# Kernel optimization log

Hardware: AMD Instinct MI355X
Metric: run time of the kernel (lower is better)

## Reference

```python
import jax, jax.numpy as jnp
import numpy as np

BLOCK = 128  # block_size in the original module


def weight_dequant(weight, scale):
    # weight: [O, I] fp8 values (simulated float32); scale: [O//BLOCK, I//BLOCK] fp32
    O, I = weight.shape
    w = weight.reshape(O // BLOCK, BLOCK, I // BLOCK, BLOCK)
    w = w * scale[:, None, :, None]
    return w.reshape(O, I)


def setup_inputs() -> dict:
    key = jax.random.key(0)
    k1, k2, k3, k4 = jax.random.split(key, 4)
    B, S, IN, OUT = 2, 2048, 4096, 16384
    x = jax.random.normal(k1, (B, S, IN), dtype=jnp.float32)
    weight = jax.random.normal(k2, (OUT, IN), dtype=jnp.float32)
    scale = jax.random.uniform(k3, (OUT // BLOCK, IN // BLOCK), dtype=jnp.float32, minval=0.01, maxval=0.05)
    bias = jax.random.normal(k4, (OUT,), dtype=jnp.float32)
    return {"x": x, "weight": weight, "scale": scale, "bias": bias}


def reference(x, weight, scale, bias):
    # bf16 gemm_impl path: block-wise dequant of fp8 weight, then F.linear(x, W) + bias
    w = weight_dequant(weight, scale)          # [O, I]
    out = jnp.einsum('bsi,oi->bso', x, w)      # x @ W^T
    return out + bias
```

## Files before the change

### kernel.cpp

```cpp
#include <hip/hip_runtime.h>
#include <hip/hip_bf16.h>

#define M_DIM 4096
#define N_DIM 16384
#define K_DIM 4096

typedef __bf16 bf16x8 __attribute__((ext_vector_type(8)));
typedef float f32x4 __attribute__((ext_vector_type(4)));

__device__ __forceinline__ void gload16(const void* g, void* l) {
    __builtin_amdgcn_global_load_lds((__attribute__((address_space(1))) void*)g,
                                     (__attribute__((address_space(3))) void*)l, 16, 0, 0);
}

__global__ __launch_bounds__(256) void cvt_x_kernel(const float* __restrict__ x,
                                                    __hip_bfloat16* __restrict__ out,
                                                    int ngroups) {
    int i = blockIdx.x * blockDim.x + threadIdx.x;
    int stride = gridDim.x * blockDim.x;
    for (; i < ngroups; i += stride) {
        const float4* p = (const float4*)(x + (size_t)i * 8);
        float4 v0 = p[0];
        float4 v1 = p[1];
        bf16x8 r;
        r[0] = (__bf16)v0.x; r[1] = (__bf16)v0.y; r[2] = (__bf16)v0.z; r[3] = (__bf16)v0.w;
        r[4] = (__bf16)v1.x; r[5] = (__bf16)v1.y; r[6] = (__bf16)v1.z; r[7] = (__bf16)v1.w;
        *(bf16x8*)(out + (size_t)i * 8) = r;
    }
}

__global__ __launch_bounds__(256) void dequant_w_kernel(const float* __restrict__ w,
                                                        const float* __restrict__ scale,
                                                        __hip_bfloat16* __restrict__ out) {
    const int ngroups = N_DIM * (K_DIM / 8);
    int i = blockIdx.x * blockDim.x + threadIdx.x;
    int stride = gridDim.x * blockDim.x;
    for (; i < ngroups; i += stride) {
        int row = i >> 9;
        int cg  = i & 511;
        float s = scale[(row >> 7) * (K_DIM / 128) + (cg >> 4)];
        const float4* p = (const float4*)(w + (size_t)i * 8);
        float4 v0 = p[0];
        float4 v1 = p[1];
        bf16x8 r;
        r[0] = (__bf16)(v0.x * s); r[1] = (__bf16)(v0.y * s);
        r[2] = (__bf16)(v0.z * s); r[3] = (__bf16)(v0.w * s);
        r[4] = (__bf16)(v1.x * s); r[5] = (__bf16)(v1.y * s);
        r[6] = (__bf16)(v1.z * s); r[7] = (__bf16)(v1.w * s);
        *(bf16x8*)(out + (size_t)i * 8) = r;
    }
}

__global__ __launch_bounds__(512, 2)
void gemm_bf16_kernel(const __hip_bfloat16* __restrict__ A,
                      const __hip_bfloat16* __restrict__ Bw,
                      const float* __restrict__ bias,
                      float* __restrict__ C) {
    constexpr int Mtiles = M_DIM / 256;
    constexpr int Ntiles = N_DIM / 256;
    constexpr int nwg = Mtiles * Ntiles;

    int bid = blockIdx.x;
    int swz = (bid & 7) * (nwg >> 3) + (bid >> 3);
    int bm = swz % Mtiles;
    int bn = swz / Mtiles;

    __shared__ bf16x8 sA[2][2048];
    __shared__ bf16x8 sB[2][2048];

    const int t = threadIdx.x;
    const int l = t & 63;
    const int w = t >> 6;
    const int wm = w >> 2;
    const int wn = w & 3;

    const int lr = l & 15;
    const int lk = l >> 4;
    const int l7 = lr & 7;

    const int s0 = lk ^ l7;
    const int s1 = (4 + lk) ^ l7;

    const int srow = w * 8 + (l >> 3);
    const int scol = ((l & 7) ^ (l >> 3)) << 3;

    const size_t K = K_DIM;
    const __hip_bfloat16* aB = A  + (size_t)(bm * 256) * K + scol;
    const __hip_bfloat16* bB = Bw + (size_t)(bn * 256) * K + scol;

    f32x4 acc[8][4] = {};

    const int arow = (wm * 128 + lr) * 8;
    const int brow = (wn * 64 + lr) * 8;

    char* A0b = (char*)&sA[0][0] + w * 1024;
    char* B0b = (char*)&sB[0][0] + w * 1024;
    char* A1b = (char*)&sA[1][0] + w * 1024;
    char* B1b = (char*)&sB[1][0] + w * 1024;

#define SH(lbase, gptr)                                                         \
    do {                                                                        \
        gload16((gptr) + (size_t)srow * K, (lbase));                            \
        gload16((gptr) + (size_t)(64 + srow) * K, (lbase) + 8192);              \
    } while (0)

#define RD_A(dst, pa_, roff)                                                    \
    _Pragma("unroll")                                                           \
    for (int mi = 0; mi < 4; ++mi) {                                            \
        dst[mi][0] = (pa_)[arow + (roff) + mi * 128 + s0];                      \
        dst[mi][1] = (pa_)[arow + (roff) + mi * 128 + s1];                      \
    }

#define RD_B(dst, pb_, roff)                                                    \
    _Pragma("unroll")                                                           \
    for (int ni = 0; ni < 2; ++ni) {                                            \
        dst[ni][0] = (pb_)[brow + (roff) + ni * 128 + s0];                      \
        dst[ni][1] = (pb_)[brow + (roff) + ni * 128 + s1];                      \
    }

#define MM(mo, no, af, bf)                                                      \
    do {                                                                        \
        __builtin_amdgcn_s_setprio(1);                                          \
        _Pragma("unroll")                                                       \
        for (int s = 0; s < 2; ++s)                                             \
            _Pragma("unroll")                                                   \
            for (int mi = 0; mi < 4; ++mi)                                      \
                _Pragma("unroll")                                               \
                for (int ni = 0; ni < 2; ++ni)                                  \
                    acc[(mo) + mi][(no) + ni] =                                 \
                        __builtin_amdgcn_mfma_f32_16x16x32_bf16(                \
                            af[mi][s], bf[ni][s], acc[(mo) + mi][(no) + ni],    \
                            0, 0, 0);                                           \
        __builtin_amdgcn_s_setprio(0);                                          \
    } while (0)

#define BAR()   __builtin_amdgcn_s_barrier()
#define SBAR()  __builtin_amdgcn_sched_barrier(0)
#define LGKM0() do { asm volatile("s_waitcnt lgkmcnt(0)" ::: "memory"); SBAR(); } while (0)

    bf16x8 a03[4][2], a47[4][2], b01[2][2], b23[2][2];
    const bf16x8* pa0 = &sA[0][0];
    const bf16x8* pb0 = &sB[0][0];
    const bf16x8* pa1 = &sA[1][0];
    const bf16x8* pb1 = &sB[1][0];

    SH(A0b, aB);  SH(A0b + 16384, aB + (size_t)128 * K);
    SH(B0b, bB);  SH(B0b + 16384, bB + (size_t)128 * K);
    SH(B1b, bB + 64);  SH(B1b + 16384, bB + 64 + (size_t)128 * K);
    asm volatile("s_waitcnt vmcnt(4)" ::: "memory");
    BAR();

    #pragma unroll 1
    for (int p = 0; p < 32; ++p) {
        const bool last = (p == 31);
        const __hip_bfloat16* gAu  = aB + (size_t)(2 * p + 1) * 64;
        const __hip_bfloat16* gAt2 = aB + (size_t)(2 * p + 2) * 64;
        const __hip_bfloat16* gBt2 = bB + (size_t)(2 * p + 2) * 64;
        const __hip_bfloat16* gBt3 = bB + (size_t)(2 * p + 3) * 64;

        RD_A(a03, pa0, 0); RD_B(b01, pb0, 0);
        SH(A1b, gAu);
        asm volatile("s_waitcnt lgkmcnt(8)" ::: "memory");
        BAR();
        LGKM0();
        MM(0, 0, a03, b01);
        BAR();
        RD_B(b23, pb0, 256);
        SH(A1b + 16384, gAu + (size_t)128 * K);
        BAR();
        LGKM0();
        MM(0, 2, a03, b23);
        BAR();
        RD_A(a47, pa0, 512);
        if (!last) SH(B0b, gBt2);
        BAR();
        LGKM0();
        MM(4, 0, a47, b01);
        BAR();
        if (!last) {
            SH(B0b + 16384, gBt2 + (size_t)128 * K);
            asm volatile("s_waitcnt vmcnt(4)" ::: "memory");
        } else {
            asm volatile("s_waitcnt vmcnt(0)" ::: "memory");
        }
        BAR();
        SBAR();
        MM(4, 2, a47, b23);
        BAR();

        RD_A(a03, pa1, 0); RD_B(b01, pb1, 0);
        if (!last) SH(A0b, gAt2);
        asm volatile("s_waitcnt lgkmcnt(8)" ::: "memory");
        BAR();
        LGKM0();
        MM(0, 0, a03, b01);
        BAR();
        RD_B(b23, pb1, 256);
        if (!last) SH(A0b + 16384, gAt2 + (size_t)128 * K);
        BAR();
        LGKM0();
        MM(0, 2, a03, b23);
        BAR();
        RD_A(a47, pa1, 512);
        if (!last) SH(B1b, gBt3);
        BAR();
        LGKM0();
        MM(4, 0, a47, b01);
        BAR();
        if (!last) {
            SH(B1b + 16384, gBt3 + (size_t)128 * K);
            asm volatile("s_waitcnt vmcnt(4)" ::: "memory");
        }
        BAR();
        SBAR();
        MM(4, 2, a47, b23);
        if (!last) BAR();
    }
#undef SH
#undef RD_A
#undef RD_B
#undef MM
#undef BAR
#undef SBAR
#undef LGKM0

    const int crow0 = bm * 256 + wm * 128;
    const int ccol0 = bn * 256 + wn * 64;
    #pragma unroll
    for (int ni = 0; ni < 4; ++ni) {
        int col = ccol0 + ni * 16 + lr;
        float bv = bias[col];
        #pragma unroll
        for (int mi = 0; mi < 8; ++mi) {
            int rbase = crow0 + mi * 16 + lk * 4;
            #pragma unroll
            for (int j = 0; j < 4; ++j) {
                C[(size_t)(rbase + j) * N_DIM + col] = acc[mi][ni][j] + bv;
            }
        }
    }
}

__global__ __launch_bounds__(256)
void gemm_fallback(const float* __restrict__ X, const float* __restrict__ W,
                   const float* __restrict__ scale, const float* __restrict__ bias,
                   float* __restrict__ C) {
    int bm = blockIdx.x % (M_DIM / 64);
    int bn = blockIdx.x / (M_DIM / 64);
    __shared__ float sA[64][33];
    __shared__ float sB[64][33];
    int t = threadIdx.x;
    int tx = t & 15, ty = t >> 4;
    float acc[4][4] = {};
    for (int kt = 0; kt < K_DIM / 32; ++kt) {
        float s = scale[(bn >> 1) * (K_DIM / 128) + (kt >> 2)];
        #pragma unroll
        for (int i = 0; i < 8; ++i) {
            int idx = t + i * 256;
            int r = idx >> 5, c = idx & 31;
            sA[r][c] = X[(size_t)(bm * 64 + r) * K_DIM + kt * 32 + c];
            sB[r][c] = W[(size_t)(bn * 64 + r) * K_DIM + kt * 32 + c] * s;
        }
        __syncthreads();
        #pragma unroll
        for (int k = 0; k < 32; ++k) {
            float a[4], b[4];
            #pragma unroll
            for (int i = 0; i < 4; ++i) a[i] = sA[ty * 4 + i][k];
            #pragma unroll
            for (int j = 0; j < 4; ++j) b[j] = sB[tx * 4 + j][k];
            #pragma unroll
            for (int i = 0; i < 4; ++i)
                #pragma unroll
                for (int j = 0; j < 4; ++j) acc[i][j] += a[i] * b[j];
        }
        __syncthreads();
    }
    #pragma unroll
    for (int i = 0; i < 4; ++i)
        #pragma unroll
        for (int j = 0; j < 4; ++j) {
            int row = bm * 64 + ty * 4 + i;
            int col = bn * 64 + tx * 4 + j;
            C[(size_t)row * N_DIM + col] = acc[i][j] + bias[col];
        }
}

extern "C" void kernel_launch(void* const* d_in, const int* in_sizes, int n_in,
                              void* d_out, int out_size, void* d_ws, size_t ws_size,
                              hipStream_t stream) {
    const float* x     = (const float*)d_in[0];
    const float* wgt   = (const float*)d_in[1];
    const float* scale = (const float*)d_in[2];
    const float* bias  = (const float*)d_in[3];
    float* out = (float*)d_out;

    const size_t need = ((size_t)M_DIM * K_DIM + (size_t)N_DIM * K_DIM) * sizeof(__hip_bfloat16);
    if (ws_size >= need) {
        __hip_bfloat16* xbf = (__hip_bfloat16*)d_ws;
        __hip_bfloat16* wbf = xbf + (size_t)M_DIM * K_DIM;
        cvt_x_kernel<<<2048, 256, 0, stream>>>(x, xbf, M_DIM * K_DIM / 8);
        dequant_w_kernel<<<4096, 256, 0, stream>>>(wgt, scale, wbf);
        gemm_bf16_kernel<<<(M_DIM / 256) * (N_DIM / 256), 512, 0, stream>>>(xbf, wbf, bias, out);
    } else {
        gemm_fallback<<<(M_DIM / 64) * (N_DIM / 64), 256, 0, stream>>>(x, wgt, scale, bias, out);
    }
}
```

Baseline: 714.0 us.

## Switch GEMM to 32x32x16 MFMA tiles and merge prep kernels

The GEMM inner loop now issues 32x32x16 bf16 MFMAs on 32-row fragments instead of 16x16x32, with a new LDS swizzle (XOR with wave index) and a re-mapped fragment read pattern and epilogue. This cuts the MFMA instruction count and LDS reads per FLOP. The two preprocessing kernels are also merged into one launch, saving a kernel launch and tail. The changed swizzle and the output row mapping risk bank conflicts or indexing errors.

```diff
diff --git a/kernel.cpp b/kernel.cpp
--- a/kernel.cpp
+++ b/kernel.cpp
@@ -6,48 +6,48 @@
 #define K_DIM 4096
 
 typedef __bf16 bf16x8 __attribute__((ext_vector_type(8)));
-typedef float f32x4 __attribute__((ext_vector_type(4)));
+typedef float f32x16 __attribute__((ext_vector_type(16)));
 
 __device__ __forceinline__ void gload16(const void* g, void* l) {
     __builtin_amdgcn_global_load_lds((__attribute__((address_space(1))) void*)g,
                                      (__attribute__((address_space(3))) void*)l, 16, 0, 0);
 }
 
-__global__ __launch_bounds__(256) void cvt_x_kernel(const float* __restrict__ x,
-                                                    __hip_bfloat16* __restrict__ out,
-                                                    int ngroups) {
-    int i = blockIdx.x * blockDim.x + threadIdx.x;
-    int stride = gridDim.x * blockDim.x;
-    for (; i < ngroups; i += stride) {
-        const float4* p = (const float4*)(x + (size_t)i * 8);
-        float4 v0 = p[0];
-        float4 v1 = p[1];
-        bf16x8 r;
-        r[0] = (__bf16)v0.x; r[1] = (__bf16)v0.y; r[2] = (__bf16)v0.z; r[3] = (__bf16)v0.w;
-        r[4] = (__bf16)v1.x; r[5] = (__bf16)v1.y; r[6] = (__bf16)v1.z; r[7] = (__bf16)v1.w;
-        *(bf16x8*)(out + (size_t)i * 8) = r;
-    }
-}
-
-__global__ __launch_bounds__(256) void dequant_w_kernel(const float* __restrict__ w,
-                                                        const float* __restrict__ scale,
-                                                        __hip_bfloat16* __restrict__ out) {
-    const int ngroups = N_DIM * (K_DIM / 8);
-    int i = blockIdx.x * blockDim.x + threadIdx.x;
-    int stride = gridDim.x * blockDim.x;
-    for (; i < ngroups; i += stride) {
-        int row = i >> 9;
-        int cg  = i & 511;
-        float s = scale[(row >> 7) * (K_DIM / 128) + (cg >> 4)];
-        const float4* p = (const float4*)(w + (size_t)i * 8);
-        float4 v0 = p[0];
-        float4 v1 = p[1];
-        bf16x8 r;
-        r[0] = (__bf16)(v0.x * s); r[1] = (__bf16)(v0.y * s);
-        r[2] = (__bf16)(v0.z * s); r[3] = (__bf16)(v0.w * s);
-        r[4] = (__bf16)(v1.x * s); r[5] = (__bf16)(v1.y * s);
-        r[6] = (__bf16)(v1.z * s); r[7] = (__bf16)(v1.w * s);
-        *(bf16x8*)(out + (size_t)i * 8) = r;
+__global__ __launch_bounds__(256) void prep_kernel(const float* __restrict__ x,
+                                                   const float* __restrict__ wgt,
+                                                   const float* __restrict__ scale,
+                                                   __hip_bfloat16* __restrict__ xbf,
+                                                   __hip_bfloat16* __restrict__ wbf) {
+    int b = blockIdx.x;
+    if (b < 2048) {
+        const int ng = M_DIM * K_DIM / 8;
+        int i = b * 256 + threadIdx.x;
+        for (; i < ng; i += 2048 * 256) {
+            const float4* p = (const float4*)(x + (size_t)i * 8);
+            float4 v0 = p[0];
+            float4 v1 = p[1];
+            bf16x8 r;
+            r[0] = (__bf16)v0.x; r[1] = (__bf16)v0.y; r[2] = (__bf16)v0.z; r[3] = (__bf16)v0.w;
+            r[4] = (__bf16)v1.x; r[5] = (__bf16)v1.y; r[6] = (__bf16)v1.z; r[7] = (__bf16)v1.w;
+            *(bf16x8*)(xbf + (size_t)i * 8) = r;
+        }
+    } else {
+        const int ng = N_DIM * (K_DIM / 8);
+        int i = (b - 2048) * 256 + threadIdx.x;
+        for (; i < ng; i += 4096 * 256) {
+            int row = i >> 9;
+            int cg  = i & 511;
+            float s = scale[(row >> 7) * (K_DIM / 128) + (cg >> 4)];
+            const float4* p = (const float4*)(wgt + (size_t)i * 8);
+            float4 v0 = p[0];
+            float4 v1 = p[1];
+            bf16x8 r;
+            r[0] = (__bf16)(v0.x * s); r[1] = (__bf16)(v0.y * s);
+            r[2] = (__bf16)(v0.z * s); r[3] = (__bf16)(v0.w * s);
+            r[4] = (__bf16)(v1.x * s); r[5] = (__bf16)(v1.y * s);
+            r[6] = (__bf16)(v1.z * s); r[7] = (__bf16)(v1.w * s);
+            *(bf16x8*)(wbf + (size_t)i * 8) = r;
+        }
     }
 }
 
@@ -74,24 +74,24 @@
     const int wm = w >> 2;
     const int wn = w & 3;
 
-    const int lr = l & 15;
-    const int lk = l >> 4;
-    const int l7 = lr & 7;
-
-    const int s0 = lk ^ l7;
-    const int s1 = (4 + lk) ^ l7;
+    const int l31 = l & 31;
+    const int lh  = l >> 5;
+    const int sig = (l & 7) ^ ((l >> 3) & 3);
+
+    const int sk[4] = { (0 + lh) ^ sig, (2 + lh) ^ sig,
+                        (4 + lh) ^ sig, (6 + lh) ^ sig };
 
     const int srow = w * 8 + (l >> 3);
-    const int scol = ((l & 7) ^ (l >> 3)) << 3;
+    const int scol = ((l & 7) ^ (l >> 3) ^ (w & 3)) << 3;
 
     const size_t K = K_DIM;
     const __hip_bfloat16* aB = A  + (size_t)(bm * 256) * K + scol;
     const __hip_bfloat16* bB = Bw + (size_t)(bn * 256) * K + scol;
 
-    f32x4 acc[8][4] = {};
-
-    const int arow = (wm * 128 + lr) * 8;
-    const int brow = (wn * 64 + lr) * 8;
+    f32x16 acc[4][2] = {};
+
+    const int arow = (wm * 128 + l31) * 8;
+    const int brow = (wn * 64 + l31) * 8;
 
     char* A0b = (char*)&sA[0][0] + w * 1024;
     char* B0b = (char*)&sB[0][0] + w * 1024;
@@ -106,31 +106,26 @@
 
 #define RD_A(dst, pa_, roff)                                                    \
     _Pragma("unroll")                                                           \
-    for (int mi = 0; mi < 4; ++mi) {                                            \
-        dst[mi][0] = (pa_)[arow + (roff) + mi * 128 + s0];                      \
-        dst[mi][1] = (pa_)[arow + (roff) + mi * 128 + s1];                      \
-    }
+    for (int sm = 0; sm < 2; ++sm)                                              \
+        _Pragma("unroll")                                                       \
+        for (int kc = 0; kc < 4; ++kc)                                          \
+            dst[sm][kc] = (pa_)[arow + (roff) + sm * 256 + sk[kc]];
 
 #define RD_B(dst, pb_, roff)                                                    \
     _Pragma("unroll")                                                           \
-    for (int ni = 0; ni < 2; ++ni) {                                            \
-        dst[ni][0] = (pb_)[brow + (roff) + ni * 128 + s0];                      \
-        dst[ni][1] = (pb_)[brow + (roff) + ni * 128 + s1];                      \
-    }
-
-#define MM(mo, no, af, bf)                                                      \
+    for (int kc = 0; kc < 4; ++kc)                                              \
+        dst[kc] = (pb_)[brow + (roff) + sk[kc]];
+
+#define MM(smb, sn, af, bf)                                                     \
     do {                                                                        \
         __builtin_amdgcn_s_setprio(1);                                          \
         _Pragma("unroll")                                                       \
-        for (int s = 0; s < 2; ++s)                                             \
+        for (int kc = 0; kc < 4; ++kc)                                          \
             _Pragma("unroll")                                                   \
-            for (int mi = 0; mi < 4; ++mi)                                      \
-                _Pragma("unroll")                                               \
-                for (int ni = 0; ni < 2; ++ni)                                  \
-                    acc[(mo) + mi][(no) + ni] =                                 \
-                        __builtin_amdgcn_mfma_f32_16x16x32_bf16(                \
-                            af[mi][s], bf[ni][s], acc[(mo) + mi][(no) + ni],    \
-                            0, 0, 0);                                           \
+            for (int sm = 0; sm < 2; ++sm)                                      \
+                acc[(smb) + sm][(sn)] =                                         \
+                    __builtin_amdgcn_mfma_f32_32x32x16_bf16(                    \
+                        af[sm][kc], bf[kc], acc[(smb) + sm][(sn)], 0, 0, 0);    \
         __builtin_amdgcn_s_setprio(0);                                          \
     } while (0)
 
@@ -138,7 +133,7 @@
 #define SBAR()  __builtin_amdgcn_sched_barrier(0)
 #define LGKM0() do { asm volatile("s_waitcnt lgkmcnt(0)" ::: "memory"); SBAR(); } while (0)
 
-    bf16x8 a03[4][2], a47[4][2], b01[2][2], b23[2][2];
+    bf16x8 aL[2][4], aH[2][4], bL[4], bH[4];
     const bf16x8* pa0 = &sA[0][0];
     const bf16x8* pb0 = &sB[0][0];
     const bf16x8* pa1 = &sA[1][0];
@@ -158,24 +153,24 @@
         const __hip_bfloat16* gBt2 = bB + (size_t)(2 * p + 2) * 64;
         const __hip_bfloat16* gBt3 = bB + (size_t)(2 * p + 3) * 64;
 
-        RD_A(a03, pa0, 0); RD_B(b01, pb0, 0);
+        RD_A(aL, pa0, 0); RD_B(bL, pb0, 0);
         SH(A1b, gAu);
         asm volatile("s_waitcnt lgkmcnt(8)" ::: "memory");
         BAR();
         LGKM0();
-        MM(0, 0, a03, b01);
-        BAR();
-        RD_B(b23, pb0, 256);
+        MM(0, 0, aL, bL);
+        BAR();
+        RD_B(bH, pb0, 256);
         SH(A1b + 16384, gAu + (size_t)128 * K);
         BAR();
         LGKM0();
-        MM(0, 2, a03, b23);
-        BAR();
-        RD_A(a47, pa0, 512);
+        MM(0, 1, aL, bH);
+        BAR();
+        RD_A(aH, pa0, 512);
         if (!last) SH(B0b, gBt2);
         BAR();
         LGKM0();
-        MM(4, 0, a47, b01);
+        MM(2, 0, aH, bL);
         BAR();
         if (!last) {
             SH(B0b + 16384, gBt2 + (size_t)128 * K);
@@ -185,27 +180,27 @@
         }
         BAR();
         SBAR();
-        MM(4, 2, a47, b23);
-        BAR();
-
-        RD_A(a03, pa1, 0); RD_B(b01, pb1, 0);
+        MM(2, 1, aH, bH);
+        BAR();
+
+        RD_A(aL, pa1, 0); RD_B(bL, pb1, 0);
         if (!last) SH(A0b, gAt2);
         asm volatile("s_waitcnt lgkmcnt(8)" ::: "memory");
         BAR();
         LGKM0();
-        MM(0, 0, a03, b01);
-        BAR();
-        RD_B(b23, pb1, 256);
+        MM(0, 0, aL, bL);
+        BAR();
+        RD_B(bH, pb1, 256);
         if (!last) SH(A0b + 16384, gAt2 + (size_t)128 * K);
         BAR();
         LGKM0();
-        MM(0, 2, a03, b23);
-        BAR();
-        RD_A(a47, pa1, 512);
+        MM(0, 1, aL, bH);
+        BAR();
+        RD_A(aH, pa1, 512);
         if (!last) SH(B1b, gBt3);
         BAR();
         LGKM0();
-        MM(4, 0, a47, b01);
+        MM(2, 0, aH, bL);
         BAR();
         if (!last) {
             SH(B1b + 16384, gBt3 + (size_t)128 * K);
@@ -213,7 +208,7 @@
         }
         BAR();
         SBAR();
-        MM(4, 2, a47, b23);
+        MM(2, 1, aH, bH);
         if (!last) BAR();
     }
 #undef SH
@@ -227,15 +222,15 @@
     const int crow0 = bm * 256 + wm * 128;
     const int ccol0 = bn * 256 + wn * 64;
     #pragma unroll
-    for (int ni = 0; ni < 4; ++ni) {
-        int col = ccol0 + ni * 16 + lr;
+    for (int sn = 0; sn < 2; ++sn) {
+        int col = ccol0 + sn * 32 + l31;
         float bv = bias[col];
         #pragma unroll
-        for (int mi = 0; mi < 8; ++mi) {
-            int rbase = crow0 + mi * 16 + lk * 4;
+        for (int sm = 0; sm < 4; ++sm) {
             #pragma unroll
-            for (int j = 0; j < 4; ++j) {
-                C[(size_t)(rbase + j) * N_DIM + col] = acc[mi][ni][j] + bv;
+            for (int reg = 0; reg < 16; ++reg) {
+                int row = crow0 + sm * 32 + (reg & 3) + 8 * (reg >> 2) + 4 * lh;
+                C[(size_t)row * N_DIM + col] = acc[sm][sn][reg] + bv;
             }
         }
     }
@@ -299,8 +294,7 @@
     if (ws_size >= need) {
         __hip_bfloat16* xbf = (__hip_bfloat16*)d_ws;
         __hip_bfloat16* wbf = xbf + (size_t)M_DIM * K_DIM;
-        cvt_x_kernel<<<2048, 256, 0, stream>>>(x, xbf, M_DIM * K_DIM / 8);
-        dequant_w_kernel<<<4096, 256, 0, stream>>>(wgt, scale, wbf);
+        prep_kernel<<<6144, 256, 0, stream>>>(x, wgt, scale, xbf, wbf);
         gemm_bf16_kernel<<<(M_DIM / 256) * (N_DIM / 256), 512, 0, stream>>>(xbf, wbf, bias, out);
     } else {
         gemm_fallback<<<(M_DIM / 64) * (N_DIM / 64), 256, 0, stream>>>(x, wgt, scale, bias, out);
```

New measurement: 702.4 us. Within noise of the previous version (-1.6%).
